# Kernel optimization log

Hardware: AMD Instinct MI355X
Metric: run time of the kernel (lower is better)

Reference implementation:

```python
import jax, jax.numpy as jnp
import numpy as np
from jax import lax

EPS = 1e-10
SIGMA_NSQ = 2.0


def _gauss_win(ws, sigma):
    # faithful to fspecial(Filter.GAUSSIAN): integer grid -ws//2+1 .. ws//2
    r = np.arange(-(ws // 2), ws // 2 + 1, dtype=np.float32)
    xx, yy = np.meshgrid(r, r, indexing='ij')
    g = np.exp(-((xx ** 2 + yy ** 2) / (2.0 * sigma ** 2))).astype(np.float32)
    eps = np.finfo(np.float32).eps
    g[g < eps * g.max()] = 0.0
    s = g.sum()
    if s != 0:
        g = g / s
    # filter2 rotates the kernel 180 deg (no-op for this symmetric Gaussian)
    g = np.rot90(g, 2).copy()
    return jnp.asarray(g)[None, None]  # [1,1,ws,ws]


def _conv_valid(img, win):
    return lax.conv_general_dilated(img, win, (1, 1), 'VALID')


def setup_inputs() -> dict:
    key = jax.random.key(0)
    k1, k2, k3 = jax.random.split(key, 3)
    B, C, H, W = 128, 3, 135, 240
    recons = jax.random.uniform(k1, (B, C, H, W), dtype=jnp.float32)
    x = jax.random.uniform(k2, (B, C, H, W), dtype=jnp.float32)
    Wlin = jax.random.normal(k3, (C * H * W, 1), dtype=jnp.float32) * 0.001
    b = jnp.zeros((1,), dtype=jnp.float32)
    return {"recons": recons, "x": x, "W": Wlin, "b": b}


def _vif(recons, x):
    # recons, x: [B, C, H, W]. NOTE: the original code computes downsampled
    # GT/P for scale>1 but never uses them, so every scale operates on the
    # full-resolution images (replicated faithfully here).
    B, C, H, W = recons.shape
    r = recons.reshape(B * C, 1, H, W)
    p = x.reshape(B * C, 1, H, W)
    num = jnp.zeros((B * C,), dtype=recons.dtype)
    den = jnp.zeros((B * C,), dtype=recons.dtype)
    for scale in range(1, 5):
        N = int(2.0 ** (4 - scale + 1) + 1)  # 17, 9, 5, 3
        win = _gauss_win(N, N / 5.0)
        mu1 = _conv_valid(r, win)
        mu2 = _conv_valid(p, win)
        GT_sum_sq = mu1 * mu1
        P_sum_sq = mu2 * mu2
        GT_P_sum_mul = mu1 * mu2
        sigmaGT_sq = _conv_valid(r * r, win) - GT_sum_sq
        sigmaP_sq = _conv_valid(p * p, win) - P_sum_sq
        sigmaGT_P = _conv_valid(r * p, win) - GT_P_sum_mul
        sigmaGT_sq = jnp.maximum(sigmaGT_sq, 0.0)
        sigmaP_sq = jnp.maximum(sigmaP_sq, 0.0)
        g = sigmaGT_P / (sigmaGT_sq + EPS)
        sv_sq = sigmaP_sq - g * sigmaGT_P
        m1 = sigmaGT_sq < EPS
        g = jnp.where(m1, 0.0, g)
        sv_sq = jnp.where(m1, sigmaP_sq, sv_sq)
        sigmaGT_sq = jnp.where(m1, 0.0, sigmaGT_sq)
        m2 = sigmaP_sq < EPS
        g = jnp.where(m2, 0.0, g)
        sv_sq = jnp.where(m2, 0.0, sv_sq)
        m3 = g < 0
        sv_sq = jnp.where(m3, sigmaP_sq, sv_sq)
        g = jnp.where(m3, 0.0, g)
        sv_sq = jnp.where(sv_sq <= EPS, EPS, sv_sq)
        num = num + jnp.sum(jnp.log10(1.0 + g * g * sigmaGT_sq / (sv_sq + SIGMA_NSQ)), axis=(1, 2, 3))
        den = den + jnp.sum(jnp.log10(1.0 + sigmaGT_sq / SIGMA_NSQ), axis=(1, 2, 3))
    vif = (num / den).reshape(B, C)
    return jnp.mean(vif, axis=1)  # per-image VIF (mean over channels)


def reference(recons, x, W, b):
    B = recons.shape[0]
    vif_per_img = _vif(recons, x)            # [B]
    recons_loss = jnp.mean(1.0 - vif_per_img)
    # base_model stand-in: flatten -> linear
    pred_recons = recons.reshape(B, -1) @ W + b
    pred_orig = x.reshape(B, -1) @ W + b
    prediction_loss = jnp.mean((pred_orig - pred_recons) ** 2)
    loss = prediction_loss + recons_loss
    return (loss, recons_loss, prediction_loss)
```

## Files before the change

### kernel.cpp

```cpp
#include <hip/hip_runtime.h>

#define Himg 135
#define Wimg 240
#define Bimg 128
#define Cimg 3
#define BCN (Bimg*Cimg)
#define HW (Himg*Wimg)
#define CHW (Cimg*HW)
#define EPSF 1e-10f
#define TOTB (BCN*2*5)

typedef float fvec4 __attribute__((ext_vector_type(4)));
typedef float f2 __attribute__((ext_vector_type(2)));
typedef float f4 __attribute__((ext_vector_type(4)));
typedef _Float16 hf;
typedef hf h2 __attribute__((ext_vector_type(2)));
typedef hf h4v __attribute__((ext_vector_type(4)));
typedef hf h8 __attribute__((ext_vector_type(8)));

#define RSTG 77
#define ASTR 72
#define RHP  104
#define APOFF 5760
#define HTOFF 11520
#define SREDO 19840
#define LDSB  39728

__device__ __forceinline__ h2 pkrtz(float a, float b) {
  return __builtin_bit_cast(h2, __builtin_amdgcn_cvt_pkrtz(a, b));
}
__device__ __forceinline__ h4v pkrtz4(float a, float b, float c, float d) {
  h2 lo = pkrtz(a, b), hi = pkrtz(c, d);
  return (h4v){lo[0], lo[1], hi[0], hi[1]};
}
__device__ __forceinline__ float aload(const float* p) {
  return __hip_atomic_load(p, __ATOMIC_RELAXED, __HIP_MEMORY_SCOPE_AGENT);
}

constexpr double cexp(double x) {
  double s = 1.0, t = 1.0;
  for (int i = 1; i < 48; ++i) { t *= x / (double)i; s += t; }
  return s;
}
template<int N>
struct GaussW {
  float inv, rsum;
  constexpr GaussW() : inv(0), rsum(0) {
    const float sig = (float)N / 5.0f;
    inv = 1.0f / (2.0f * sig * sig);
    float ssum = 0.f;
    for (int i = 0; i < N; ++i) {
      float d = (float)(i - N / 2);
      ssum += (float)cexp((double)(-(d * d) * inv));
    }
    rsum = 1.0f / ssum;
  }
};


template<int N>
__device__ __forceinline__ void scale_pass(
    int chunk, int band, const hf* Ar, const hf* Ap, hf* Ht,
    int ln, int quad, int wave, float& numAcc, float& denAcc)
{
  constexpr int OW  = Wimg - N + 1;
  constexpr int OV  = Himg - N + 1;
  constexpr int OV0 = (OV + 1) / 2;
  constexpr int TIL = (OV0 + 15) / 16;
  constexpr int THT = TIL + 1;
  constexpr int NHT = (THT + 3) / 4;
  constexpr int NVT = (TIL + 3) / 4;
  constexpr GaussW<N> GW{};

  const int OVc  = chunk ? (OV - OV0) : OV0;
  const int hoff = chunk ? (OV0 - 58) : 0;
  const f4 zf = {0.f, 0.f, 0.f, 0.f};

  h8 wfrag;
  #pragma unroll
  for (int j = 0; j < 8; ++j) {
    const int di = quad * 8 + j - ln;
    const float fd = (float)(di - N / 2);
    float v = __expf(-(fd * fd) * GW.inv) * GW.rsum;
    v = ((unsigned)di < (unsigned)N) ? v : 0.f;
    wfrag[j] = (hf)v;
  }

  for (int ct = 0; ct < 3; ++ct) {
    __syncthreads();
    #pragma unroll
    for (int i = 0; i < NHT; ++i) {
      const int t = wave + i * 4;
      if (t < THT) {
        int rowL = hoff + t * 16 + ln;
        if (rowL > RSTG - 1) rowL = RSTG - 1;
        const int ao = rowL * ASTR + ct * 16 + quad * 8;
        h8 ra = *(const h8*)(Ar + ao);
        h8 pa = *(const h8*)(Ap + ao);
        h8 rsq = ra * ra, psq = pa * pa, rp = ra * pa;
        f4 d0 = __builtin_amdgcn_mfma_f32_16x16x32_f16(ra,  wfrag, zf, 0, 0, 0);
        f4 d1 = __builtin_amdgcn_mfma_f32_16x16x32_f16(pa,  wfrag, zf, 0, 0, 0);
        f4 d2 = __builtin_amdgcn_mfma_f32_16x16x32_f16(rsq, wfrag, zf, 0, 0, 0);
        f4 d3 = __builtin_amdgcn_mfma_f32_16x16x32_f16(psq, wfrag, zf, 0, 0, 0);
        f4 d4 = __builtin_amdgcn_mfma_f32_16x16x32_f16(rp,  wfrag, zf, 0, 0, 0);
        hf* hb = Ht + (ln * 5) * RHP + t * 16 + quad * 4;
        *(h4v*)(hb + 0 * RHP) = pkrtz4(d0[0], d0[1], d0[2], d0[3]);
        *(h4v*)(hb + 1 * RHP) = pkrtz4(d1[0], d1[1], d1[2], d1[3]);
        *(h4v*)(hb + 2 * RHP) = pkrtz4(d2[0], d2[1], d2[2], d2[3]);
        *(h4v*)(hb + 3 * RHP) = pkrtz4(d3[0], d3[1], d3[2], d3[3]);
        *(h4v*)(hb + 4 * RHP) = pkrtz4(d4[0], d4[1], d4[2], d4[3]);
      }
    }
    __syncthreads();
    const int ocol = band * 48 + ct * 16 + ln;
    const bool colv = ocol < OW;
    #pragma unroll
    for (int i = 0; i < NVT; ++i) {
      const int v = wave + i * 4;
      if (v < TIL) {
        const int j0 = v * 16;
        f4 C[5];
        #pragma unroll
        for (int c = 0; c < 5; ++c) {
          h8 bf = *(const h8*)(Ht + (ln * 5 + c) * RHP + j0 + quad * 8);
          C[c] = __builtin_amdgcn_mfma_f32_16x16x32_f16(wfrag, bf, zf, 0, 0, 0);
        }
        float numP = 1.f, denP = 1.f;
        const f2 z2 = {0.f, 0.f};
        #pragma unroll
        for (int pr2 = 0; pr2 < 2; ++pr2) {
          f2 mu1 = {C[0][2 * pr2], C[0][2 * pr2 + 1]};
          f2 mu2 = {C[1][2 * pr2], C[1][2 * pr2 + 1]};
          f2 m2c = {C[2][2 * pr2], C[2][2 * pr2 + 1]};
          f2 m3c = {C[3][2 * pr2], C[3][2 * pr2 + 1]};
          f2 m4c = {C[4][2 * pr2], C[4][2 * pr2 + 1]};
          f2 sGT = __builtin_elementwise_max(m2c - mu1 * mu1, z2);
          f2 sP  = __builtin_elementwise_max(m3c - mu2 * mu2, z2);
          f2 sGP = m4c - mu1 * mu2;
          f2 A   = sGT + EPSF;
          f2 t1  = sGP * sGP;
          f2 D   = A * __builtin_elementwise_fma(sP + 2.f, A, -t1);
          f2 rn  = t1 * sGT;
          #pragma unroll
          for (int e = 0; e < 2; ++e) {
            const int reg = pr2 * 2 + e;
            const int orow = j0 + quad * 4 + reg;
            const bool inb = (orow < OVc) && colv;
            float numf = 1.f + __fdividef(rn[e], D[e]);
            const bool valid = inb && (fminf(sGT[e], sP[e]) >= EPSF) && (sGP[e] > 0.f);
            numf = valid ? numf : 1.f;
            float denf = inb ? fmaf(sGT[e], 0.5f, 1.f) : 1.f;
            numP *= numf;
            denP *= denf;
          }
        }
        numAcc += __log10f(numP);
        denAcc += __log10f(denP);
      }
    }
  }
}

__global__ __launch_bounds__(256, 4) void vif_fat_kernel(
    const float* __restrict__ recons, const float* __restrict__ xim,
    const float* __restrict__ Wl, float* __restrict__ ws,
    float* __restrict__ out)
{
  extern __shared__ hf lds[];
  hf* Ar = lds;
  hf* Ap = lds + APOFF;
  hf* Ht = lds + HTOFF;
  float* sred = (float*)(lds + SREDO);

  const int b     = blockIdx.x;
  const int band  = b % 5;
  const int rest  = b / 5;
  const int chunk = rest & 1;
  const int bc    = rest >> 1;
  const int img   = bc / 3;
  const int tid   = threadIdx.x;
  const int lane  = tid & 63;
  const int ln    = lane & 15;
  const int quad  = lane >> 4;
  const int wave  = tid >> 6;
  const int r0s   = chunk ? 58 : 0;

  const float* rb = recons + bc * HW;
  const float* pb = xim + bc * HW;
  const float* wb = Wl + (bc % 3) * HW;

  float dotAcc = 0.f;
  #pragma unroll
  for (int i = 0; i < 3; ++i) {
    const int it = tid + i * 256;
    if (it < RSTG * 8) {
      const int row = it >> 3;
      const int c8  = it & 7;
      const int grow = r0s + row;
      int gcol = band * 48 + c8 * 8;
      if (gcol > Wimg - 8) gcol = Wimg - 8;
      const int idx = grow * Wimg + gcol;
      fvec4 r0 = *(const fvec4*)(rb + idx);
      fvec4 r1 = *(const fvec4*)(rb + idx + 4);
      fvec4 p0 = *(const fvec4*)(pb + idx);
      fvec4 p1 = *(const fvec4*)(pb + idx + 4);
      h2 a0 = pkrtz(r0[0], r0[1]), a1 = pkrtz(r0[2], r0[3]);
      h2 a2 = pkrtz(r1[0], r1[1]), a3 = pkrtz(r1[2], r1[3]);
      h2 b0 = pkrtz(p0[0], p0[1]), b1 = pkrtz(p0[2], p0[3]);
      h2 b2 = pkrtz(p1[0], p1[1]), b3 = pkrtz(p1[2], p1[3]);
      *(h8*)(Ar + row * ASTR + c8 * 8) =
          (h8){a0[0], a0[1], a1[0], a1[1], a2[0], a2[1], a3[0], a3[1]};
      *(h8*)(Ap + row * ASTR + c8 * 8) =
          (h8){b0[0], b0[1], b1[0], b1[1], b2[0], b2[1], b3[0], b3[1]};
      const bool rowOwned = chunk ? (grow >= 68) : (grow < 68);
      if (c8 < 6 && rowOwned) {
        fvec4 w0 = *(const fvec4*)(wb + idx);
        fvec4 w1 = *(const fvec4*)(wb + idx + 4);
        dotAcc += (p0[0]-r0[0])*w0[0] + (p0[1]-r0[1])*w0[1]
                + (p0[2]-r0[2])*w0[2] + (p0[3]-r0[3])*w0[3]
                + (p1[0]-r1[0])*w1[0] + (p1[1]-r1[1])*w1[1]
                + (p1[2]-r1[2])*w1[2] + (p1[3]-r1[3])*w1[3];
      }
    }
  }

  float numAcc = 0.f, denAcc = 0.f;
  scale_pass<17>(chunk, band, Ar, Ap, Ht, ln, quad, wave, numAcc, denAcc);
  scale_pass< 9>(chunk, band, Ar, Ap, Ht, ln, quad, wave, numAcc, denAcc);
  scale_pass< 5>(chunk, band, Ar, Ap, Ht, ln, quad, wave, numAcc, denAcc);
  scale_pass< 3>(chunk, band, Ar, Ap, Ht, ln, quad, wave, numAcc, denAcc);

  #pragma unroll
  for (int off = 32; off > 0; off >>= 1) {
    numAcc += __shfl_down(numAcc, off);
    denAcc += __shfl_down(denAcc, off);
    dotAcc += __shfl_down(dotAcc, off);
  }
  __syncthreads();
  if (lane == 0) {
    sred[wave] = numAcc; sred[4 + wave] = denAcc; sred[8 + wave] = dotAcc;
  }
  __syncthreads();
  if (tid == 0) {
    atomicAdd(&ws[bc],        sred[0] + sred[1] + sred[2] + sred[3]);
    atomicAdd(&ws[384 + bc],  sred[4] + sred[5] + sred[6] + sred[7]);
    atomicAdd(&ws[768 + img], sred[8] + sred[9] + sred[10] + sred[11]);
    asm volatile("s_waitcnt vmcnt(0)" ::: "memory");
    unsigned old = atomicAdd((unsigned*)(ws + 896), 1u);
    sred[0] = (old == TOTB - 1) ? 1.f : 0.f;
  }
  __syncthreads();
  if (sred[0] == 0.f) return;

  asm volatile("" ::: "memory");
  float* s1 = (float*)lds;
  float* s2 = s1 + 128;
  if (tid < 128) {
    float d = aload(ws + 768 + tid);
    float psq = d * d;
    float vimg = 0.f;
    #pragma unroll
    for (int c = 0; c < 3; ++c) {
      const int bcx = tid * 3 + c;
      vimg += aload(ws + bcx) / aload(ws + 384 + bcx);
    }
    float rl = 1.f - vimg * (1.f / 3.f);
    s1[tid] = psq; s2[tid] = rl;
  }
  __syncthreads();
  for (int off = 64; off > 0; off >>= 1) {
    if (tid < off) { s1[tid] += s1[tid + off]; s2[tid] += s2[tid + off]; }
    __syncthreads();
  }
  if (tid == 0) {
    float pred = s1[0] * (1.f / 128.f);
    float rec  = s2[0] * (1.f / 128.f);
    out[0] = pred + rec;
    out[1] = rec;
    out[2] = pred;
  }
}

extern "C" void kernel_launch(void* const* d_in, const int* in_sizes, int n_in,
                              void* d_out, int out_size, void* d_ws, size_t ws_size,
                              hipStream_t stream) {
  const float* recons = (const float*)d_in[0];
  const float* x      = (const float*)d_in[1];
  const float* Wl     = (const float*)d_in[2];
  float* ws  = (float*)d_ws;
  float* out = (float*)d_out;

  hipMemsetAsync(d_ws, 0, 904 * sizeof(float), stream);

  vif_fat_kernel<<<TOTB, 256, LDSB, stream>>>(recons, x, Wl, ws, out);
}
```

Measured before the change: 203.8 us.

## Give each wave private column jobs with rolling horizontal tiles, removing block barriers

```diff
diff --git a/kernel.cpp b/kernel.cpp
--- a/kernel.cpp
+++ b/kernel.cpp
@@ -19,12 +19,12 @@
 typedef hf h8 __attribute__((ext_vector_type(8)));
 
 #define RSTG 77
-#define ASTR 72
-#define RHP  104
-#define APOFF 5760
-#define HTOFF 11520
-#define SREDO 19840
-#define LDSB  39728
+#define ASTR 64
+#define APOFF 4928
+#define HT0   9856
+#define HTWSZ 2560
+#define SREDO 20096
+#define LDSB  40240
 
 __device__ __forceinline__ h2 pkrtz(float a, float b) {
   return __builtin_bit_cast(h2, __builtin_amdgcn_cvt_pkrtz(a, b));
@@ -59,17 +59,16 @@
 
 
 template<int N>
-__device__ __forceinline__ void scale_pass(
-    int chunk, int band, const hf* Ar, const hf* Ap, hf* Ht,
-    int ln, int quad, int wave, float& numAcc, float& denAcc)
+__device__ __forceinline__ void job_col(
+    int ct, int chunk, int band, const hf* __restrict__ Ar,
+    const hf* __restrict__ Ap, hf* __restrict__ HtW,
+    int ln, int quad, float& numAcc, float& denAcc)
 {
   constexpr int OW  = Wimg - N + 1;
   constexpr int OV  = Himg - N + 1;
   constexpr int OV0 = (OV + 1) / 2;
   constexpr int TIL = (OV0 + 15) / 16;
   constexpr int THT = TIL + 1;
-  constexpr int NHT = (THT + 3) / 4;
-  constexpr int NVT = (TIL + 3) / 4;
   constexpr GaussW<N> GW{};
 
   const int OVc  = chunk ? (OV - OV0) : OV0;
@@ -86,78 +85,78 @@
     wfrag[j] = (hf)v;
   }
 
-  for (int ct = 0; ct < 3; ++ct) {
-    __syncthreads();
+  const int swz  = (ln & 7) << 3;
+  const int ocol = band * 48 + ct * 16 + ln;
+  const bool colv = ocol < OW;
+
+  auto htile = [&](int t) {
+    int rowL = hoff + t * 16 + ln;
+    if (rowL > RSTG - 1) rowL = RSTG - 1;
+    const int ao = (rowL * ASTR + ct * 16 + quad * 8) ^ ((rowL & 7) << 3);
+    h8 ra = *(const h8*)(Ar + ao);
+    h8 pa = *(const h8*)(Ap + ao);
+    h8 rsq = ra * ra, psq = pa * pa, rp = ra * pa;
+    f4 d0 = __builtin_amdgcn_mfma_f32_16x16x32_f16(ra,  wfrag, zf, 0, 0, 0);
+    f4 d1 = __builtin_amdgcn_mfma_f32_16x16x32_f16(pa,  wfrag, zf, 0, 0, 0);
+    f4 d2 = __builtin_amdgcn_mfma_f32_16x16x32_f16(rsq, wfrag, zf, 0, 0, 0);
+    f4 d3 = __builtin_amdgcn_mfma_f32_16x16x32_f16(psq, wfrag, zf, 0, 0, 0);
+    f4 d4 = __builtin_amdgcn_mfma_f32_16x16x32_f16(rp,  wfrag, zf, 0, 0, 0);
+    const int wb = ln * 160 + (t & 1) * 16 + quad * 4;
+    *(h4v*)(HtW + ((wb + 0 * 32) ^ swz)) = pkrtz4(d0[0], d0[1], d0[2], d0[3]);
+    *(h4v*)(HtW + ((wb + 1 * 32) ^ swz)) = pkrtz4(d1[0], d1[1], d1[2], d1[3]);
+    *(h4v*)(HtW + ((wb + 2 * 32) ^ swz)) = pkrtz4(d2[0], d2[1], d2[2], d2[3]);
+    *(h4v*)(HtW + ((wb + 3 * 32) ^ swz)) = pkrtz4(d3[0], d3[1], d3[2], d3[3]);
+    *(h4v*)(HtW + ((wb + 4 * 32) ^ swz)) = pkrtz4(d4[0], d4[1], d4[2], d4[3]);
+  };
+
+  auto vtile = [&](int v) {
+    const int j0 = v * 16;
+    const int slot  = (v + (quad >> 1)) & 1;
+    const int rbase = ln * 160 + slot * 16 + 8 * (quad & 1);
+    f4 C[5];
     #pragma unroll
-    for (int i = 0; i < NHT; ++i) {
-      const int t = wave + i * 4;
-      if (t < THT) {
-        int rowL = hoff + t * 16 + ln;
-        if (rowL > RSTG - 1) rowL = RSTG - 1;
-        const int ao = rowL * ASTR + ct * 16 + quad * 8;
-        h8 ra = *(const h8*)(Ar + ao);
-        h8 pa = *(const h8*)(Ap + ao);
-        h8 rsq = ra * ra, psq = pa * pa, rp = ra * pa;
-        f4 d0 = __builtin_amdgcn_mfma_f32_16x16x32_f16(ra,  wfrag, zf, 0, 0, 0);
-        f4 d1 = __builtin_amdgcn_mfma_f32_16x16x32_f16(pa,  wfrag, zf, 0, 0, 0);
-        f4 d2 = __builtin_amdgcn_mfma_f32_16x16x32_f16(rsq, wfrag, zf, 0, 0, 0);
-        f4 d3 = __builtin_amdgcn_mfma_f32_16x16x32_f16(psq, wfrag, zf, 0, 0, 0);
-        f4 d4 = __builtin_amdgcn_mfma_f32_16x16x32_f16(rp,  wfrag, zf, 0, 0, 0);
-        hf* hb = Ht + (ln * 5) * RHP + t * 16 + quad * 4;
-        *(h4v*)(hb + 0 * RHP) = pkrtz4(d0[0], d0[1], d0[2], d0[3]);
-        *(h4v*)(hb + 1 * RHP) = pkrtz4(d1[0], d1[1], d1[2], d1[3]);
-        *(h4v*)(hb + 2 * RHP) = pkrtz4(d2[0], d2[1], d2[2], d2[3]);
-        *(h4v*)(hb + 3 * RHP) = pkrtz4(d3[0], d3[1], d3[2], d3[3]);
-        *(h4v*)(hb + 4 * RHP) = pkrtz4(d4[0], d4[1], d4[2], d4[3]);
+    for (int c = 0; c < 5; ++c) {
+      h8 bf = *(const h8*)(HtW + ((rbase + c * 32) ^ swz));
+      C[c] = __builtin_amdgcn_mfma_f32_16x16x32_f16(wfrag, bf, zf, 0, 0, 0);
+    }
+    float numP = 1.f, denP = 1.f;
+    const f2 z2 = {0.f, 0.f};
+    #pragma unroll
+    for (int pr2 = 0; pr2 < 2; ++pr2) {
+      f2 mu1 = {C[0][2 * pr2], C[0][2 * pr2 + 1]};
+      f2 mu2 = {C[1][2 * pr2], C[1][2 * pr2 + 1]};
+      f2 m2c = {C[2][2 * pr2], C[2][2 * pr2 + 1]};
+      f2 m3c = {C[3][2 * pr2], C[3][2 * pr2 + 1]};
+      f2 m4c = {C[4][2 * pr2], C[4][2 * pr2 + 1]};
+      f2 sGT = __builtin_elementwise_max(m2c - mu1 * mu1, z2);
+      f2 sP  = __builtin_elementwise_max(m3c - mu2 * mu2, z2);
+      f2 sGP = m4c - mu1 * mu2;
+      f2 A   = sGT + EPSF;
+      f2 t1  = sGP * sGP;
+      f2 D   = A * __builtin_elementwise_fma(sP + 2.f, A, -t1);
+      f2 rn  = t1 * sGT;
+      #pragma unroll
+      for (int e = 0; e < 2; ++e) {
+        const int reg = pr2 * 2 + e;
+        const int orow = j0 + quad * 4 + reg;
+        const bool inb = (orow < OVc) && colv;
+        float numf = 1.f + __fdividef(rn[e], D[e]);
+        const bool valid = inb && (fminf(sGT[e], sP[e]) >= EPSF) && (sGP[e] > 0.f);
+        numf = valid ? numf : 1.f;
+        float denf = inb ? fmaf(sGT[e], 0.5f, 1.f) : 1.f;
+        numP *= numf;
+        denP *= denf;
       }
     }
-    __syncthreads();
-    const int ocol = band * 48 + ct * 16 + ln;
-    const bool colv = ocol < OW;
-    #pragma unroll
-    for (int i = 0; i < NVT; ++i) {
-      const int v = wave + i * 4;
-      if (v < TIL) {
-        const int j0 = v * 16;
-        f4 C[5];
-        #pragma unroll
-        for (int c = 0; c < 5; ++c) {
-          h8 bf = *(const h8*)(Ht + (ln * 5 + c) * RHP + j0 + quad * 8);
-          C[c] = __builtin_amdgcn_mfma_f32_16x16x32_f16(wfrag, bf, zf, 0, 0, 0);
-        }
-        float numP = 1.f, denP = 1.f;
-        const f2 z2 = {0.f, 0.f};
-        #pragma unroll
-        for (int pr2 = 0; pr2 < 2; ++pr2) {
-          f2 mu1 = {C[0][2 * pr2], C[0][2 * pr2 + 1]};
-          f2 mu2 = {C[1][2 * pr2], C[1][2 * pr2 + 1]};
-          f2 m2c = {C[2][2 * pr2], C[2][2 * pr2 + 1]};
-          f2 m3c = {C[3][2 * pr2], C[3][2 * pr2 + 1]};
-          f2 m4c = {C[4][2 * pr2], C[4][2 * pr2 + 1]};
-          f2 sGT = __builtin_elementwise_max(m2c - mu1 * mu1, z2);
-          f2 sP  = __builtin_elementwise_max(m3c - mu2 * mu2, z2);
-          f2 sGP = m4c - mu1 * mu2;
-          f2 A   = sGT + EPSF;
-          f2 t1  = sGP * sGP;
-          f2 D   = A * __builtin_elementwise_fma(sP + 2.f, A, -t1);
-          f2 rn  = t1 * sGT;
-          #pragma unroll
-          for (int e = 0; e < 2; ++e) {
-            const int reg = pr2 * 2 + e;
-            const int orow = j0 + quad * 4 + reg;
-            const bool inb = (orow < OVc) && colv;
-            float numf = 1.f + __fdividef(rn[e], D[e]);
-            const bool valid = inb && (fminf(sGT[e], sP[e]) >= EPSF) && (sGP[e] > 0.f);
-            numf = valid ? numf : 1.f;
-            float denf = inb ? fmaf(sGT[e], 0.5f, 1.f) : 1.f;
-            numP *= numf;
-            denP *= denf;
-          }
-        }
-        numAcc += __log10f(numP);
-        denAcc += __log10f(denP);
-      }
-    }
+    numAcc += __log10f(numP);
+    denAcc += __log10f(denP);
+  };
+
+  htile(0);
+  #pragma unroll
+  for (int v = 0; v < TIL; ++v) {
+    htile(v + 1);
+    vtile(v);
   }
 }
 
@@ -169,7 +168,6 @@
   extern __shared__ hf lds[];
   hf* Ar = lds;
   hf* Ap = lds + APOFF;
-  hf* Ht = lds + HTOFF;
   float* sred = (float*)(lds + SREDO);
 
   const int b     = blockIdx.x;
@@ -184,6 +182,8 @@
   const int quad  = lane >> 4;
   const int wave  = tid >> 6;
   const int r0s   = chunk ? 58 : 0;
+
+  hf* HtW = lds + HT0 + wave * HTWSZ;
 
   const float* rb = recons + bc * HW;
   const float* pb = xim + bc * HW;
@@ -208,9 +208,10 @@
       h2 a2 = pkrtz(r1[0], r1[1]), a3 = pkrtz(r1[2], r1[3]);
       h2 b0 = pkrtz(p0[0], p0[1]), b1 = pkrtz(p0[2], p0[3]);
       h2 b2 = pkrtz(p1[0], p1[1]), b3 = pkrtz(p1[2], p1[3]);
-      *(h8*)(Ar + row * ASTR + c8 * 8) =
+      const int wo = (row * ASTR + c8 * 8) ^ ((row & 7) << 3);
+      *(h8*)(Ar + wo) =
           (h8){a0[0], a0[1], a1[0], a1[1], a2[0], a2[1], a3[0], a3[1]};
-      *(h8*)(Ap + row * ASTR + c8 * 8) =
+      *(h8*)(Ap + wo) =
           (h8){b0[0], b0[1], b1[0], b1[1], b2[0], b2[1], b3[0], b3[1]};
       const bool rowOwned = chunk ? (grow >= 68) : (grow < 68);
       if (c8 < 6 && rowOwned) {
@@ -223,12 +224,26 @@
       }
     }
   }
+  __syncthreads();
 
   float numAcc = 0.f, denAcc = 0.f;
-  scale_pass<17>(chunk, band, Ar, Ap, Ht, ln, quad, wave, numAcc, denAcc);
-  scale_pass< 9>(chunk, band, Ar, Ap, Ht, ln, quad, wave, numAcc, denAcc);
-  scale_pass< 5>(chunk, band, Ar, Ap, Ht, ln, quad, wave, numAcc, denAcc);
-  scale_pass< 3>(chunk, band, Ar, Ap, Ht, ln, quad, wave, numAcc, denAcc);
+  if (wave == 0) {
+    job_col<17>(0, chunk, band, Ar, Ap, HtW, ln, quad, numAcc, denAcc);
+    job_col<17>(1, chunk, band, Ar, Ap, HtW, ln, quad, numAcc, denAcc);
+    job_col< 5>(0, chunk, band, Ar, Ap, HtW, ln, quad, numAcc, denAcc);
+  } else if (wave == 1) {
+    job_col<17>(2, chunk, band, Ar, Ap, HtW, ln, quad, numAcc, denAcc);
+    job_col< 9>(0, chunk, band, Ar, Ap, HtW, ln, quad, numAcc, denAcc);
+    job_col< 5>(1, chunk, band, Ar, Ap, HtW, ln, quad, numAcc, denAcc);
+  } else if (wave == 2) {
+    job_col< 9>(1, chunk, band, Ar, Ap, HtW, ln, quad, numAcc, denAcc);
+    job_col< 5>(2, chunk, band, Ar, Ap, HtW, ln, quad, numAcc, denAcc);
+    job_col< 3>(0, chunk, band, Ar, Ap, HtW, ln, quad, numAcc, denAcc);
+  } else {
+    job_col< 9>(2, chunk, band, Ar, Ap, HtW, ln, quad, numAcc, denAcc);
+    job_col< 3>(1, chunk, band, Ar, Ap, HtW, ln, quad, numAcc, denAcc);
+    job_col< 3>(2, chunk, band, Ar, Ap, HtW, ln, quad, numAcc, denAcc);
+  }
 
   #pragma unroll
   for (int off = 32; off > 0; off >>= 1) {
```

Result: slower. 222.1 us (+9.0%).
